# Kernel optimization log

Measured on AMD Instinct MI355X. Metric: run time of the kernel, lower is better.

## Reference

```python
import jax, jax.numpy as jnp
import numpy as np

NUM_ROUNDS = 2
NUM_REVERSE_ROUNDS = 2


def _scatter_mean(x, src, dst, n):
    # PyG mean aggregation: out[i] = mean_{(src->i) in E} x[src]; 0 if no in-edges.
    deg = jax.ops.segment_sum(jnp.ones((src.shape[0],), x.dtype), dst, num_segments=n)
    s = jax.ops.segment_sum(x[src], dst, num_segments=n)
    return s / jnp.maximum(deg, 1.0)[:, None]


def setup_inputs() -> dict:
    key = jax.random.key(0)
    ks = jax.random.split(key, 12)
    N_TEXT, N_NON, E, EMB, R = 100000, 10000, 500000, 256, 500
    N = N_TEXT + N_NON
    PRED_IN = 4 * EMB + 2 * 2 + 2 * 2 * (NUM_ROUNDS + NUM_REVERSE_ROUNDS)  # 1044
    return {
        "h_id_tensor": jax.random.randint(ks[0], (E,), 0, N),
        "r_id_tensor": jax.random.randint(ks[1], (E,), 0, R),
        "t_id_tensor": jax.random.randint(ks[2], (E,), 0, N),
        "q_emb": jax.random.normal(ks[3], (EMB,), jnp.float32),
        "entity_embs": jax.random.normal(ks[4], (N_TEXT, EMB), jnp.float32),
        "num_non_text_entities": N_NON,
        "relation_embs": jax.random.normal(ks[5], (R, EMB), jnp.float32),
        "topic_entity_one_hot": jax.random.uniform(ks[6], (N, 2), jnp.float32),
        "non_text_emb": jax.random.normal(ks[7], (1, EMB), jnp.float32),
        "W1": jax.random.normal(ks[8], (PRED_IN, EMB), jnp.float32) * 0.02,
        "b1": jnp.zeros((EMB,), jnp.float32),
        "W2": jax.random.normal(ks[9], (EMB, 1), jnp.float32) * 0.02,
        "b2": jnp.zeros((1,), jnp.float32),
    }


def reference(h_id_tensor, r_id_tensor, t_id_tensor, q_emb, entity_embs,
              num_non_text_entities, relation_embs, topic_entity_one_hot,
              non_text_emb, W1, b1, W2, b2):
    n = entity_embs.shape[0] + num_non_text_entities
    # h_e base: text entity embs + broadcast non-text embedding
    h_e0 = jnp.concatenate(
        [entity_embs, jnp.broadcast_to(non_text_emb, (num_non_text_entities, non_text_emb.shape[1]))],
        axis=0)
    h_e_list = [h_e0, topic_entity_one_hot]
    # DDE forward rounds: messages flow h_id -> t_id
    h_pe = topic_entity_one_hot
    for _ in range(NUM_ROUNDS):
        h_pe = _scatter_mean(h_pe, h_id_tensor, t_id_tensor, n)
        h_e_list.append(h_pe)
    # reverse rounds: messages flow t_id -> h_id
    h_pe = topic_entity_one_hot
    for _ in range(NUM_REVERSE_ROUNDS):
        h_pe = _scatter_mean(h_pe, t_id_tensor, h_id_tensor, n)
        h_e_list.append(h_pe)
    h_e = jnp.concatenate(h_e_list, axis=1)  # [N, emb + 2 + 2*(R+Rr)]
    e = h_id_tensor.shape[0]
    h_triple = jnp.concatenate(
        [jnp.broadcast_to(q_emb[None, :], (e, q_emb.shape[0])),
         h_e[h_id_tensor],
         relation_embs[r_id_tensor],
         h_e[t_id_tensor]], axis=1)  # [E, 1044]
    hidden = jax.nn.relu(h_triple @ W1 + b1)
    return hidden @ W2 + b2
```

## Files before the change

kernel.cpp:

```cpp
#include <hip/hip_runtime.h>
#include <stdint.h>

#define EMB 256
#define LDK 288
#define DDE 10
#define EU  4

typedef __attribute__((ext_vector_type(8))) short short8;
typedef __attribute__((ext_vector_type(4))) float f32x4;

__device__ __forceinline__ unsigned short f2bf(float f) {
    union { float f; unsigned int u; } v; v.f = f;
    unsigned int u = v.u;
    unsigned int r = (u + 0x7FFFu + ((u >> 16) & 1u)) >> 16;
    return (unsigned short)r;
}
__device__ __forceinline__ float bf2f(unsigned short b) {
    union { unsigned int u; float f; } v; v.u = ((unsigned int)b) << 16;
    return v.f;
}

#define FPSCALE 1048576.0f
#define FPINV   (1.0f / 1048576.0f)

__device__ __forceinline__ unsigned long long pack2(float a, float b) {
    unsigned int ua = (unsigned int)(a * FPSCALE);
    unsigned int ub = (unsigned int)(b * FPSCALE);
    return ((unsigned long long)ua << 36) | ((unsigned long long)ub << 10);
}


__global__ void k_r1_fused(const int* __restrict__ h_id, const int* __restrict__ t_id,
                           const float2* __restrict__ topic,
                           unsigned long long* __restrict__ fwd,
                           unsigned long long* __restrict__ rev, int E, int SC1,
                           const float4* __restrict__ entity, const float4* __restrict__ nontext,
                           ushort4* __restrict__ he4, int n_text, int N) {
    int b = blockIdx.x;
    if (b < SC1) {
        int e = b * 256 + threadIdx.x;
        if (e >= E) return;
        int h = h_id[e], t = t_id[e];
        float2 th = topic[h];
        float2 tt = topic[t];
        atomicAdd(&fwd[t], pack2(th.x, th.y) | 1ULL);
        atomicAdd(&rev[h], pack2(tt.x, tt.y) | 1ULL);
    } else {
        int idx = (b - SC1) * 256 + threadIdx.x;
        int n = idx >> 6, q = idx & 63;
        float4 v = make_float4(0.f, 0.f, 0.f, 0.f);
        if (n < N) v = (n < n_text) ? entity[(size_t)n * 64 + q] : nontext[q];
        he4[(size_t)n * (LDK / 4) + q] = make_ushort4(f2bf(v.x), f2bf(v.y), f2bf(v.z), f2bf(v.w));
    }
}

__global__ void k_norm1(const unsigned long long* __restrict__ fwd,
                        const unsigned long long* __restrict__ rev,
                        float2* __restrict__ d1n, float2* __restrict__ r1n, int N) {
    int n = blockIdx.x * blockDim.x + threadIdx.x;
    if (n >= N) return;
    unsigned long long f = fwd[n], r = rev[n];
    float df = fmaxf((float)(f & 0x3FFULL), 1.0f);
    float dr = fmaxf((float)(r & 0x3FFULL), 1.0f);
    d1n[n] = make_float2((float)((f >> 36) & 0x3FFFFFFULL) * FPINV / df,
                         (float)((f >> 10) & 0x3FFFFFFULL) * FPINV / df);
    r1n[n] = make_float2((float)((r >> 36) & 0x3FFFFFFULL) * FPINV / dr,
                         (float)((r >> 10) & 0x3FFFFFFULL) * FPINV / dr);
}


__global__ void k_r2_fused(const int* __restrict__ h_id, const int* __restrict__ t_id,
                           const float2* __restrict__ d1n, const float2* __restrict__ r1n,
                           unsigned long long* __restrict__ s2,
                           unsigned long long* __restrict__ sr2, int E, int SC2, int WT_BLK,
                           const float* __restrict__ W1,
                           unsigned short* __restrict__ wT,
                           const float* __restrict__ qv, const float* __restrict__ rel,
                           const float* __restrict__ b1, unsigned short* __restrict__ Prb) {
    int b = blockIdx.x;
    if (b < SC2) {
        int e = b * 256 + threadIdx.x;
        if (e >= E) return;
        int h = h_id[e], t = t_id[e];
        float2 dh = d1n[h];
        float2 rt = r1n[t];
        atomicAdd(&s2[t], pack2(dh.x, dh.y));
        atomicAdd(&sr2[h], pack2(rt.x, rt.y));
    } else if (b < SC2 + WT_BLK) {
        int idx = (b - SC2) * 256 + threadIdx.x;
        int j = idx / LDK;
        int k = idx - j * LDK;
        int col   = (j < EMB) ? j : (j - EMB);
        int baseE = (j < EMB) ? 256 : 778;
        int baseD = (j < EMB) ? 512 : 1034;
        float v = 0.0f;
        if (k < EMB)            v = W1[(long long)(baseE + k) * EMB + col];
        else if (k < EMB + DDE) v = W1[(long long)(baseD + (k - EMB)) * EMB + col];
        wT[idx] = f2bf(v);
    } else {
        int r = b - SC2 - WT_BLK;
        int j = threadIdx.x;
        float acc = b1[j];
        for (int k = 0; k < EMB; ++k)
            acc = fmaf(qv[k], W1[(long long)k * EMB + j], acc);
        const float* relr = rel + (long long)r * EMB;
        for (int k = 0; k < EMB; ++k)
            acc = fmaf(relr[k], W1[(long long)(522 + k) * EMB + j], acc);
        Prb[(long long)r * EMB + j] = f2bf(acc);
    }
}

__global__ void k_norm2(const unsigned long long* __restrict__ fwd,
                        const unsigned long long* __restrict__ rev,
                        const unsigned long long* __restrict__ s2,
                        const unsigned long long* __restrict__ sr2,
                        float2* __restrict__ d2n, float2* __restrict__ r2n, int N) {
    int n = blockIdx.x * blockDim.x + threadIdx.x;
    if (n >= N) return;
    float df = fmaxf((float)(fwd[n] & 0x3FFULL), 1.0f);
    float dr = fmaxf((float)(rev[n] & 0x3FFULL), 1.0f);
    unsigned long long a = s2[n], b = sr2[n];
    d2n[n] = make_float2((float)((a >> 36) & 0x3FFFFFFULL) * FPINV / df,
                         (float)((a >> 10) & 0x3FFFFFFULL) * FPINV / df);
    r2n[n] = make_float2((float)((b >> 36) & 0x3FFFFFFULL) * FPINV / dr,
                         (float)((b >> 10) & 0x3FFFFFFULL) * FPINV / dr);
}

__global__ void k_he_tail(const float2* __restrict__ topic,
                          const float2* __restrict__ d1, const float2* __restrict__ d2,
                          const float2* __restrict__ r1, const float2* __restrict__ r2,
                          ushort4* __restrict__ he4, int N, int Mpad) {
    int idx = blockIdx.x * blockDim.x + threadIdx.x;
    if (idx >= Mpad * 8) return;
    int n = idx >> 3, j = idx & 7;
    float4 v = make_float4(0.f, 0.f, 0.f, 0.f);
    if (n < N) {
        if (j == 0)      { float2 a = topic[n], bq = d1[n]; v = make_float4(a.x, a.y, bq.x, bq.y); }
        else if (j == 1) { float2 a = d2[n],   bq = r1[n]; v = make_float4(a.x, a.y, bq.x, bq.y); }
        else if (j == 2) { float2 a = r2[n];               v = make_float4(a.x, a.y, 0.f, 0.f); }
    }
    he4[(size_t)n * (LDK / 4) + 64 + j] = make_ushort4(f2bf(v.x), f2bf(v.y), f2bf(v.z), f2bf(v.w));
}

__global__ __launch_bounds__(512) void k_gemm(const unsigned short* __restrict__ he,
                                              const unsigned short* __restrict__ wT,
                                              unsigned short* __restrict__ Ph,
                                              unsigned short* __restrict__ Pt) {
    __shared__ __align__(16) unsigned short lA[128 * 32];
    __shared__ __align__(16) unsigned short lB[256 * 32];
    const int t = threadIdx.x;
    const int lane = t & 63;
    const int w = t >> 6;
    const int br = blockIdx.x >> 1;
    const int bc = blockIdx.x & 1;
    const int wr = w >> 2;
    const int wc = w & 3;

    f32x4 acc[4][4];
#pragma unroll
    for (int r = 0; r < 4; ++r)
#pragma unroll
        for (int c = 0; c < 4; ++c)
            acc[r][c] = (f32x4){0.f, 0.f, 0.f, 0.f};

    const char* baseA = (const char*)he + (size_t)(br * 128) * (LDK * 2);
    const char* baseB = (const char*)wT + (size_t)(bc * 256) * (LDK * 2);

    const int rowX = t >> 2;
    const int colb = (t & 3) * 16;

    for (int k0 = 0; k0 < LDK; k0 += 32) {
        __syncthreads();
        {
            const char* srcA  = baseA + (size_t)rowX * (LDK * 2) + k0 * 2 + colb;
            const char* srcB0 = baseB + (size_t)rowX * (LDK * 2) + k0 * 2 + colb;
            const char* srcB1 = baseB + (size_t)(rowX + 128) * (LDK * 2) + k0 * 2 + colb;
            __builtin_amdgcn_global_load_lds((const __attribute__((address_space(1))) void*)srcA,
                                             (__attribute__((address_space(3))) void*)((char*)lA + t * 16), 16, 0, 0);
            __builtin_amdgcn_global_load_lds((const __attribute__((address_space(1))) void*)srcB0,
                                             (__attribute__((address_space(3))) void*)((char*)lB + t * 16), 16, 0, 0);
            __builtin_amdgcn_global_load_lds((const __attribute__((address_space(1))) void*)srcB1,
                                             (__attribute__((address_space(3))) void*)((char*)lB + 8192 + t * 16), 16, 0, 0);
        }
        __syncthreads();

        short8 af[4], bfr[4];
#pragma unroll
        for (int r = 0; r < 4; ++r) {
            int arow = wr * 64 + r * 16 + (lane & 15);
            af[r] = *(const short8*)(lA + arow * 32 + (lane >> 4) * 8);
        }
#pragma unroll
        for (int c = 0; c < 4; ++c) {
            int brow = wc * 64 + c * 16 + (lane & 15);
            bfr[c] = *(const short8*)(lB + brow * 32 + (lane >> 4) * 8);
        }
#pragma unroll
        for (int r = 0; r < 4; ++r)
#pragma unroll
            for (int c = 0; c < 4; ++c)
                acc[r][c] = __builtin_amdgcn_mfma_f32_16x16x32_bf16(af[r], bfr[c], acc[r][c], 0, 0, 0);
    }

    unsigned short* Pout = bc ? Pt : Ph;
    const int nbase = wc * 64;
    const int mbase = br * 128 + wr * 64 + (lane >> 4) * 4;
#pragma unroll
    for (int r = 0; r < 4; ++r) {
#pragma unroll
        for (int c = 0; c < 4; ++c) {
            int n = nbase + c * 16 + (lane & 15);
#pragma unroll
            for (int i = 0; i < 4; ++i) {
                int m = mbase + r * 16 + i;
                Pout[(size_t)m * EMB + n] = f2bf(acc[r][c][i]);
            }
        }
    }
}

__global__ __launch_bounds__(256) void k_edge(
    const int* __restrict__ h_id, const int* __restrict__ r_id, const int* __restrict__ t_id,
    const unsigned short* __restrict__ Ph, const unsigned short* __restrict__ Pt,
    const unsigned short* __restrict__ Prb, const float* __restrict__ W2,
    const float* __restrict__ b2, float* __restrict__ out, int E) {
    const int lane = threadIdx.x & 63;
    const int gw = (blockIdx.x * blockDim.x + threadIdx.x) >> 6;
    const int nw = (gridDim.x * blockDim.x) >> 6;
    float4 w2 = *(const float4*)(W2 + 4 * lane);
    float bb = b2[0];
    const int lo = 4 * lane;

    for (int e0 = gw * EU; e0 < E; e0 += nw * EU) {
        if (e0 + EU <= E) {
            int h[EU], r[EU], t[EU];
#pragma unroll
            for (int u = 0; u < EU; ++u) {
                h[u] = h_id[e0 + u]; r[u] = r_id[e0 + u]; t[u] = t_id[e0 + u];
            }
            ushort4 ph[EU], pt[EU], pr[EU];
#pragma unroll
            for (int u = 0; u < EU; ++u) {
                ph[u] = *(const ushort4*)(Ph + (size_t)h[u] * EMB + lo);
                pt[u] = *(const ushort4*)(Pt + (size_t)t[u] * EMB + lo);
                pr[u] = *(const ushort4*)(Prb + (size_t)r[u] * EMB + lo);
            }
#pragma unroll
            for (int u = 0; u < EU; ++u) {
                float v, acc;
                v = bf2f(pr[u].x) + bf2f(ph[u].x) + bf2f(pt[u].x); acc  = fmaxf(v, 0.f) * w2.x;
                v = bf2f(pr[u].y) + bf2f(ph[u].y) + bf2f(pt[u].y); acc += fmaxf(v, 0.f) * w2.y;
                v = bf2f(pr[u].z) + bf2f(ph[u].z) + bf2f(pt[u].z); acc += fmaxf(v, 0.f) * w2.z;
                v = bf2f(pr[u].w) + bf2f(ph[u].w) + bf2f(pt[u].w); acc += fmaxf(v, 0.f) * w2.w;
#pragma unroll
                for (int m = 32; m >= 1; m >>= 1) acc += __shfl_xor(acc, m, 64);
                if (lane == 0) out[e0 + u] = acc + bb;
            }
        } else {
            for (int u = 0; u < E - e0; ++u) {
                int h = h_id[e0 + u], rr = r_id[e0 + u], tt = t_id[e0 + u];
                ushort4 ph = *(const ushort4*)(Ph + (size_t)h * EMB + lo);
                ushort4 pt = *(const ushort4*)(Pt + (size_t)tt * EMB + lo);
                ushort4 pr = *(const ushort4*)(Prb + (size_t)rr * EMB + lo);
                float v, acc;
                v = bf2f(pr.x) + bf2f(ph.x) + bf2f(pt.x); acc  = fmaxf(v, 0.f) * w2.x;
                v = bf2f(pr.y) + bf2f(ph.y) + bf2f(pt.y); acc += fmaxf(v, 0.f) * w2.y;
                v = bf2f(pr.z) + bf2f(ph.z) + bf2f(pt.z); acc += fmaxf(v, 0.f) * w2.z;
                v = bf2f(pr.w) + bf2f(ph.w) + bf2f(pt.w); acc += fmaxf(v, 0.f) * w2.w;
#pragma unroll
                for (int m = 32; m >= 1; m >>= 1) acc += __shfl_xor(acc, m, 64);
                if (lane == 0) out[e0 + u] = acc + bb;
            }
        }
    }
}


extern "C" void kernel_launch(void* const* d_in, const int* in_sizes, int n_in,
                              void* d_out, int out_size, void* d_ws, size_t ws_size,
                              hipStream_t stream) {
    const int*   h_id    = (const int*)d_in[0];
    const int*   r_id    = (const int*)d_in[1];
    const int*   t_id    = (const int*)d_in[2];
    const float* q       = (const float*)d_in[3];
    const float* entity  = (const float*)d_in[4];
    const float* rel     = (const float*)d_in[6];
    const float* topic   = (const float*)d_in[7];
    const float* nontext = (const float*)d_in[8];
    const float* W1      = (const float*)d_in[9];
    const float* b1      = (const float*)d_in[10];
    const float* W2      = (const float*)d_in[11];
    const float* b2      = (const float*)d_in[12];

    const int E      = in_sizes[0];
    const int n_text = in_sizes[4] / EMB;
    const int N      = in_sizes[7] / 2;
    const int R      = in_sizes[6] / EMB;
    const int Mpad   = (N + 127) & ~127;

    char* p = (char*)d_ws;
    auto alloc = [&](size_t bytes) {
        char* r = p;
        p += (bytes + 255) & ~(size_t)255;
        return r;
    };
    unsigned long long* fwd = (unsigned long long*)alloc((size_t)Mpad * 8);
    unsigned long long* rev = (unsigned long long*)alloc((size_t)Mpad * 8);
    unsigned long long* s2  = (unsigned long long*)alloc((size_t)Mpad * 8);
    unsigned long long* sr2 = (unsigned long long*)alloc((size_t)Mpad * 8);
    size_t zero_bytes = (size_t)(p - (char*)d_ws);
    float2* d1n = (float2*)alloc((size_t)Mpad * 8);
    float2* r1n = (float2*)alloc((size_t)Mpad * 8);
    float2* d2n = (float2*)alloc((size_t)Mpad * 8);
    float2* r2n = (float2*)alloc((size_t)Mpad * 8);
    unsigned short* he  = (unsigned short*)alloc((size_t)Mpad * LDK * 2);
    unsigned short* wT  = (unsigned short*)alloc((size_t)512 * LDK * 2);
    unsigned short* Prb = (unsigned short*)alloc((size_t)R * EMB * 2);
    unsigned short* Ph  = (unsigned short*)alloc((size_t)Mpad * EMB * 2);
    unsigned short* Pt  = (unsigned short*)alloc((size_t)Mpad * EMB * 2);

    hipMemsetAsync(d_ws, 0, zero_bytes, stream);

    const int T = 256;
    const int SC1 = (E + T - 1) / T;
    const int COPY_BLK = Mpad / 4;
    const int SC2 = SC1;
    const int WT_BLK = (512 * LDK) / T;

    k_r1_fused<<<SC1 + COPY_BLK, T, 0, stream>>>(
        h_id, t_id, (const float2*)topic, fwd, rev, E, SC1,
        (const float4*)entity, (const float4*)nontext, (ushort4*)he, n_text, N);
    k_norm1<<<(Mpad + T - 1) / T, T, 0, stream>>>(fwd, rev, d1n, r1n, Mpad);
    k_r2_fused<<<SC2 + WT_BLK + R, T, 0, stream>>>(
        h_id, t_id, d1n, r1n, s2, sr2, E, SC2, WT_BLK, W1, wT, q, rel, b1, Prb);
    k_norm2<<<(Mpad + T - 1) / T, T, 0, stream>>>(fwd, rev, s2, sr2, d2n, r2n, Mpad);
    k_he_tail<<<(Mpad * 8 + T - 1) / T, T, 0, stream>>>(
        (const float2*)topic, d1n, d2n, r1n, r2n, (ushort4*)he, N, Mpad);

    k_gemm<<<(Mpad / 128) * 2, 512, 0, stream>>>(he, wT, Ph, Pt);

    k_edge<<<2048, T, 0, stream>>>(h_id, r_id, t_id, Ph, Pt, Prb, W2, b2, (float*)d_out, E);
}
```

Measured before the change: 305.3 us.

## Fold normalization kernels into consumers and widen per-lane edge gathers

Removes the two normalization kernels by decoding the packed fixed-point sums directly in the round-2 scatter and tail kernels, and moves the weight transpose and relation-bias precompute into the first fused launch. This cuts the launch count from seven to five and drops the intermediate float2 buffers. The edge kernel now gives each half-wavefront one edge, with 16-byte nontemporal loads, a 32-lane reduction and a doubled grid. In exchange the packed values are decoded redundantly per edge, and the first launch becomes larger and more mixed.

```diff
diff --git a/kernel.cpp b/kernel.cpp
--- a/kernel.cpp
+++ b/kernel.cpp
@@ -4,10 +4,10 @@
 #define EMB 256
 #define LDK 288
 #define DDE 10
-#define EU  4
 
 typedef __attribute__((ext_vector_type(8))) short short8;
 typedef __attribute__((ext_vector_type(4))) float f32x4;
+typedef __attribute__((ext_vector_type(4))) int int4v;
 
 __device__ __forceinline__ unsigned short f2bf(float f) {
     union { float f; unsigned int u; } v; v.f = f;
@@ -28,14 +28,26 @@
     unsigned int ub = (unsigned int)(b * FPSCALE);
     return ((unsigned long long)ua << 36) | ((unsigned long long)ub << 10);
 }
+__device__ __forceinline__ float2 unpack2(unsigned long long v) {
+    float d = fmaxf((float)(unsigned int)(v & 0x3FFULL), 1.0f);
+    return make_float2((float)((v >> 36) & 0x3FFFFFFULL) * FPINV / d,
+                       (float)((v >> 10) & 0x3FFFFFFULL) * FPINV / d);
+}
+__device__ __forceinline__ float2 unpack2d(unsigned long long v, float d) {
+    return make_float2((float)((v >> 36) & 0x3FFFFFFULL) * FPINV / d,
+                       (float)((v >> 10) & 0x3FFFFFFULL) * FPINV / d);
+}
 
 
 __global__ void k_r1_fused(const int* __restrict__ h_id, const int* __restrict__ t_id,
                            const float2* __restrict__ topic,
                            unsigned long long* __restrict__ fwd,
-                           unsigned long long* __restrict__ rev, int E, int SC1,
+                           unsigned long long* __restrict__ rev, int E, int SC1, int COPY, int WT_BLK,
                            const float4* __restrict__ entity, const float4* __restrict__ nontext,
-                           ushort4* __restrict__ he4, int n_text, int N) {
+                           ushort4* __restrict__ he4, int n_text, int N,
+                           const float* __restrict__ W1, unsigned short* __restrict__ wT,
+                           const float* __restrict__ qv, const float* __restrict__ rel,
+                           const float* __restrict__ b1, unsigned short* __restrict__ Prb) {
     int b = blockIdx.x;
     if (b < SC1) {
         int e = b * 256 + threadIdx.x;
@@ -45,49 +57,14 @@
         float2 tt = topic[t];
         atomicAdd(&fwd[t], pack2(th.x, th.y) | 1ULL);
         atomicAdd(&rev[h], pack2(tt.x, tt.y) | 1ULL);
-    } else {
+    } else if (b < SC1 + COPY) {
         int idx = (b - SC1) * 256 + threadIdx.x;
         int n = idx >> 6, q = idx & 63;
         float4 v = make_float4(0.f, 0.f, 0.f, 0.f);
         if (n < N) v = (n < n_text) ? entity[(size_t)n * 64 + q] : nontext[q];
         he4[(size_t)n * (LDK / 4) + q] = make_ushort4(f2bf(v.x), f2bf(v.y), f2bf(v.z), f2bf(v.w));
-    }
-}
-
-__global__ void k_norm1(const unsigned long long* __restrict__ fwd,
-                        const unsigned long long* __restrict__ rev,
-                        float2* __restrict__ d1n, float2* __restrict__ r1n, int N) {
-    int n = blockIdx.x * blockDim.x + threadIdx.x;
-    if (n >= N) return;
-    unsigned long long f = fwd[n], r = rev[n];
-    float df = fmaxf((float)(f & 0x3FFULL), 1.0f);
-    float dr = fmaxf((float)(r & 0x3FFULL), 1.0f);
-    d1n[n] = make_float2((float)((f >> 36) & 0x3FFFFFFULL) * FPINV / df,
-                         (float)((f >> 10) & 0x3FFFFFFULL) * FPINV / df);
-    r1n[n] = make_float2((float)((r >> 36) & 0x3FFFFFFULL) * FPINV / dr,
-                         (float)((r >> 10) & 0x3FFFFFFULL) * FPINV / dr);
-}
-
-
-__global__ void k_r2_fused(const int* __restrict__ h_id, const int* __restrict__ t_id,
-                           const float2* __restrict__ d1n, const float2* __restrict__ r1n,
-                           unsigned long long* __restrict__ s2,
-                           unsigned long long* __restrict__ sr2, int E, int SC2, int WT_BLK,
-                           const float* __restrict__ W1,
-                           unsigned short* __restrict__ wT,
-                           const float* __restrict__ qv, const float* __restrict__ rel,
-                           const float* __restrict__ b1, unsigned short* __restrict__ Prb) {
-    int b = blockIdx.x;
-    if (b < SC2) {
-        int e = b * 256 + threadIdx.x;
-        if (e >= E) return;
-        int h = h_id[e], t = t_id[e];
-        float2 dh = d1n[h];
-        float2 rt = r1n[t];
-        atomicAdd(&s2[t], pack2(dh.x, dh.y));
-        atomicAdd(&sr2[h], pack2(rt.x, rt.y));
-    } else if (b < SC2 + WT_BLK) {
-        int idx = (b - SC2) * 256 + threadIdx.x;
+    } else if (b < SC1 + COPY + WT_BLK) {
+        int idx = (b - SC1 - COPY) * 256 + threadIdx.x;
         int j = idx / LDK;
         int k = idx - j * LDK;
         int col   = (j < EMB) ? j : (j - EMB);
@@ -98,7 +75,7 @@
         else if (k < EMB + DDE) v = W1[(long long)(baseD + (k - EMB)) * EMB + col];
         wT[idx] = f2bf(v);
     } else {
-        int r = b - SC2 - WT_BLK;
+        int r = b - SC1 - COPY - WT_BLK;
         int j = threadIdx.x;
         float acc = b1[j];
         for (int k = 0; k < EMB; ++k)
@@ -110,34 +87,47 @@
     }
 }
 
-__global__ void k_norm2(const unsigned long long* __restrict__ fwd,
-                        const unsigned long long* __restrict__ rev,
-                        const unsigned long long* __restrict__ s2,
-                        const unsigned long long* __restrict__ sr2,
-                        float2* __restrict__ d2n, float2* __restrict__ r2n, int N) {
-    int n = blockIdx.x * blockDim.x + threadIdx.x;
-    if (n >= N) return;
-    float df = fmaxf((float)(fwd[n] & 0x3FFULL), 1.0f);
-    float dr = fmaxf((float)(rev[n] & 0x3FFULL), 1.0f);
-    unsigned long long a = s2[n], b = sr2[n];
-    d2n[n] = make_float2((float)((a >> 36) & 0x3FFFFFFULL) * FPINV / df,
-                         (float)((a >> 10) & 0x3FFFFFFULL) * FPINV / df);
-    r2n[n] = make_float2((float)((b >> 36) & 0x3FFFFFFULL) * FPINV / dr,
-                         (float)((b >> 10) & 0x3FFFFFFULL) * FPINV / dr);
-}
-
-__global__ void k_he_tail(const float2* __restrict__ topic,
-                          const float2* __restrict__ d1, const float2* __restrict__ d2,
-                          const float2* __restrict__ r1, const float2* __restrict__ r2,
-                          ushort4* __restrict__ he4, int N, int Mpad) {
+
+__global__ void k_r2(const int* __restrict__ h_id, const int* __restrict__ t_id,
+                     const unsigned long long* __restrict__ fwd,
+                     const unsigned long long* __restrict__ rev,
+                     unsigned long long* __restrict__ s2,
+                     unsigned long long* __restrict__ sr2, int E) {
+    int e = blockIdx.x * blockDim.x + threadIdx.x;
+    if (e >= E) return;
+    int h = h_id[e], t = t_id[e];
+    float2 dh = unpack2(fwd[h]);
+    float2 rt = unpack2(rev[t]);
+    atomicAdd(&s2[t], pack2(dh.x, dh.y));
+    atomicAdd(&sr2[h], pack2(rt.x, rt.y));
+}
+
+
+__global__ void k_tail(const float2* __restrict__ topic,
+                       const unsigned long long* __restrict__ fwd,
+                       const unsigned long long* __restrict__ rev,
+                       const unsigned long long* __restrict__ s2,
+                       const unsigned long long* __restrict__ sr2,
+                       ushort4* __restrict__ he4, int N, int Mpad) {
     int idx = blockIdx.x * blockDim.x + threadIdx.x;
     if (idx >= Mpad * 8) return;
     int n = idx >> 3, j = idx & 7;
     float4 v = make_float4(0.f, 0.f, 0.f, 0.f);
-    if (n < N) {
-        if (j == 0)      { float2 a = topic[n], bq = d1[n]; v = make_float4(a.x, a.y, bq.x, bq.y); }
-        else if (j == 1) { float2 a = d2[n],   bq = r1[n]; v = make_float4(a.x, a.y, bq.x, bq.y); }
-        else if (j == 2) { float2 a = r2[n];               v = make_float4(a.x, a.y, 0.f, 0.f); }
+    if (n < N && j < 3) {
+        if (j == 0) {
+            float2 a = topic[n];
+            float2 b = unpack2(fwd[n]);
+            v = make_float4(a.x, a.y, b.x, b.y);
+        } else if (j == 1) {
+            float df = fmaxf((float)(unsigned int)(fwd[n] & 0x3FFULL), 1.0f);
+            float2 a = unpack2d(s2[n], df);
+            float2 b = unpack2(rev[n]);
+            v = make_float4(a.x, a.y, b.x, b.y);
+        } else {
+            float dr = fmaxf((float)(unsigned int)(rev[n] & 0x3FFULL), 1.0f);
+            float2 a = unpack2d(sr2[n], dr);
+            v = make_float4(a.x, a.y, 0.f, 0.f);
+        }
     }
     he4[(size_t)n * (LDK / 4) + 64 + j] = make_ushort4(f2bf(v.x), f2bf(v.y), f2bf(v.z), f2bf(v.w));
 }
@@ -219,58 +209,53 @@
     }
 }
 
+__device__ __forceinline__ short8 ntload(const unsigned short* p) {
+    union { int4v i; short8 s; } u;
+    u.i = __builtin_nontemporal_load((const int4v*)p);
+    return u.s;
+}
+
 __global__ __launch_bounds__(256) void k_edge(
     const int* __restrict__ h_id, const int* __restrict__ r_id, const int* __restrict__ t_id,
     const unsigned short* __restrict__ Ph, const unsigned short* __restrict__ Pt,
     const unsigned short* __restrict__ Prb, const float* __restrict__ W2,
     const float* __restrict__ b2, float* __restrict__ out, int E) {
     const int lane = threadIdx.x & 63;
+    const int half = lane >> 5;
+    const int l32  = lane & 31;
     const int gw = (blockIdx.x * blockDim.x + threadIdx.x) >> 6;
     const int nw = (gridDim.x * blockDim.x) >> 6;
-    float4 w2 = *(const float4*)(W2 + 4 * lane);
-    float bb = b2[0];
-    const int lo = 4 * lane;
-
-    for (int e0 = gw * EU; e0 < E; e0 += nw * EU) {
-        if (e0 + EU <= E) {
-            int h[EU], r[EU], t[EU];
-#pragma unroll
-            for (int u = 0; u < EU; ++u) {
-                h[u] = h_id[e0 + u]; r[u] = r_id[e0 + u]; t[u] = t_id[e0 + u];
+    const int lo = l32 * 8;
+    float w2v[8];
+    *(float4*)&w2v[0] = *(const float4*)(W2 + lo);
+    *(float4*)&w2v[4] = *(const float4*)(W2 + lo + 4);
+    const float bb = b2[0];
+
+    for (int e0 = gw * 4; e0 < E; e0 += nw * 4) {
+        short8 ph[2], pt[2], pr[2];
+        int ev[2];
+#pragma unroll
+        for (int p = 0; p < 2; ++p) {
+            int e = e0 + 2 * p + half;
+            ev[p] = e;
+            int ec = (e < E) ? e : 0;
+            int h = h_id[ec], r = r_id[ec], t = t_id[ec];
+            ph[p] = ntload(Ph + (size_t)h * EMB + lo);
+            pt[p] = ntload(Pt + (size_t)t * EMB + lo);
+            pr[p] = *(const short8*)(Prb + (size_t)r * EMB + lo);
+        }
+#pragma unroll
+        for (int p = 0; p < 2; ++p) {
+            float acc = 0.f;
+#pragma unroll
+            for (int j = 0; j < 8; ++j) {
+                float v = bf2f((unsigned short)pr[p][j]) + bf2f((unsigned short)ph[p][j])
+                        + bf2f((unsigned short)pt[p][j]);
+                acc += fmaxf(v, 0.f) * w2v[j];
             }
-            ushort4 ph[EU], pt[EU], pr[EU];
-#pragma unroll
-            for (int u = 0; u < EU; ++u) {
-                ph[u] = *(const ushort4*)(Ph + (size_t)h[u] * EMB + lo);
-                pt[u] = *(const ushort4*)(Pt + (size_t)t[u] * EMB + lo);
-                pr[u] = *(const ushort4*)(Prb + (size_t)r[u] * EMB + lo);
-            }
-#pragma unroll
-            for (int u = 0; u < EU; ++u) {
-                float v, acc;
-                v = bf2f(pr[u].x) + bf2f(ph[u].x) + bf2f(pt[u].x); acc  = fmaxf(v, 0.f) * w2.x;
-                v = bf2f(pr[u].y) + bf2f(ph[u].y) + bf2f(pt[u].y); acc += fmaxf(v, 0.f) * w2.y;
-                v = bf2f(pr[u].z) + bf2f(ph[u].z) + bf2f(pt[u].z); acc += fmaxf(v, 0.f) * w2.z;
-                v = bf2f(pr[u].w) + bf2f(ph[u].w) + bf2f(pt[u].w); acc += fmaxf(v, 0.f) * w2.w;
-#pragma unroll
-                for (int m = 32; m >= 1; m >>= 1) acc += __shfl_xor(acc, m, 64);
-                if (lane == 0) out[e0 + u] = acc + bb;
-            }
-        } else {
-            for (int u = 0; u < E - e0; ++u) {
-                int h = h_id[e0 + u], rr = r_id[e0 + u], tt = t_id[e0 + u];
-                ushort4 ph = *(const ushort4*)(Ph + (size_t)h * EMB + lo);
-                ushort4 pt = *(const ushort4*)(Pt + (size_t)tt * EMB + lo);
-                ushort4 pr = *(const ushort4*)(Prb + (size_t)rr * EMB + lo);
-                float v, acc;
-                v = bf2f(pr.x) + bf2f(ph.x) + bf2f(pt.x); acc  = fmaxf(v, 0.f) * w2.x;
-                v = bf2f(pr.y) + bf2f(ph.y) + bf2f(pt.y); acc += fmaxf(v, 0.f) * w2.y;
-                v = bf2f(pr.z) + bf2f(ph.z) + bf2f(pt.z); acc += fmaxf(v, 0.f) * w2.z;
-                v = bf2f(pr.w) + bf2f(ph.w) + bf2f(pt.w); acc += fmaxf(v, 0.f) * w2.w;
-#pragma unroll
-                for (int m = 32; m >= 1; m >>= 1) acc += __shfl_xor(acc, m, 64);
-                if (lane == 0) out[e0 + u] = acc + bb;
-            }
+#pragma unroll
+            for (int m = 16; m >= 1; m >>= 1) acc += __shfl_xor(acc, m, 64);
+            if (l32 == 0 && ev[p] < E) out[ev[p]] = acc + bb;
         }
     }
 }
@@ -309,10 +294,6 @@
     unsigned long long* s2  = (unsigned long long*)alloc((size_t)Mpad * 8);
     unsigned long long* sr2 = (unsigned long long*)alloc((size_t)Mpad * 8);
     size_t zero_bytes = (size_t)(p - (char*)d_ws);
-    float2* d1n = (float2*)alloc((size_t)Mpad * 8);
-    float2* r1n = (float2*)alloc((size_t)Mpad * 8);
-    float2* d2n = (float2*)alloc((size_t)Mpad * 8);
-    float2* r2n = (float2*)alloc((size_t)Mpad * 8);
     unsigned short* he  = (unsigned short*)alloc((size_t)Mpad * LDK * 2);
     unsigned short* wT  = (unsigned short*)alloc((size_t)512 * LDK * 2);
     unsigned short* Prb = (unsigned short*)alloc((size_t)R * EMB * 2);
@@ -323,21 +304,18 @@
 
     const int T = 256;
     const int SC1 = (E + T - 1) / T;
-    const int COPY_BLK = Mpad / 4;
-    const int SC2 = SC1;
+    const int COPY = Mpad / 4;
     const int WT_BLK = (512 * LDK) / T;
 
-    k_r1_fused<<<SC1 + COPY_BLK, T, 0, stream>>>(
-        h_id, t_id, (const float2*)topic, fwd, rev, E, SC1,
-        (const float4*)entity, (const float4*)nontext, (ushort4*)he, n_text, N);
-    k_norm1<<<(Mpad + T - 1) / T, T, 0, stream>>>(fwd, rev, d1n, r1n, Mpad);
-    k_r2_fused<<<SC2 + WT_BLK + R, T, 0, stream>>>(
-        h_id, t_id, d1n, r1n, s2, sr2, E, SC2, WT_BLK, W1, wT, q, rel, b1, Prb);
-    k_norm2<<<(Mpad + T - 1) / T, T, 0, stream>>>(fwd, rev, s2, sr2, d2n, r2n, Mpad);
-    k_he_tail<<<(Mpad * 8 + T - 1) / T, T, 0, stream>>>(
-        (const float2*)topic, d1n, d2n, r1n, r2n, (ushort4*)he, N, Mpad);
+    k_r1_fused<<<SC1 + COPY + WT_BLK + R, T, 0, stream>>>(
+        h_id, t_id, (const float2*)topic, fwd, rev, E, SC1, COPY, WT_BLK,
+        (const float4*)entity, (const float4*)nontext, (ushort4*)he, n_text, N,
+        W1, wT, q, rel, b1, Prb);
+    k_r2<<<SC1, T, 0, stream>>>(h_id, t_id, fwd, rev, s2, sr2, E);
+    k_tail<<<(Mpad * 8 + T - 1) / T, T, 0, stream>>>(
+        (const float2*)topic, fwd, rev, s2, sr2, (ushort4*)he, N, Mpad);
 
     k_gemm<<<(Mpad / 128) * 2, 512, 0, stream>>>(he, wT, Ph, Pt);
 
-    k_edge<<<2048, T, 0, stream>>>(h_id, r_id, t_id, Ph, Pt, Prb, W2, b2, (float*)d_out, E);
-}
+    k_edge<<<4096, T, 0, stream>>>(h_id, r_id, t_id, Ph, Pt, Prb, W2, b2, (float*)d_out, E);
+}
```

After: 312.9 us. +2.5%, slower.
